# Performance work log

Measured on AMD Instinct MI355X. Metric: run time of the kernel, lower is better.

Reference implementation:

```python
import jax, jax.numpy as jnp
import numpy as np

B, D_IN, HID, LAT, K = 8192, 1024, 2048, 256, 4096

def setup_inputs() -> dict:
    key = jax.random.key(0)
    ks = jax.random.split(key, 16)
    s = lambda fan_in: 1.0 / np.sqrt(fan_in)
    inp = {
        'x':  jax.random.normal(ks[0], (B, D_IN), jnp.float32),
        # encoder MLP
        'W1': jax.random.normal(ks[1], (D_IN, HID), jnp.float32) * s(D_IN),
        'b1': jnp.zeros((HID,), jnp.float32),
        'W2': jax.random.normal(ks[2], (HID, HID), jnp.float32) * s(HID),
        'b2': jnp.zeros((HID,), jnp.float32),
        'W3': jax.random.normal(ks[3], (HID, LAT), jnp.float32) * s(HID),
        'b3': jnp.zeros((LAT,), jnp.float32),
        # codebook, uniform(-1/K, 1/K) per nn.init.uniform_
        'embed': jax.random.uniform(ks[4], (K, LAT), jnp.float32, -1.0 / K, 1.0 / K),
        # decoder MLP
        'D1': jax.random.normal(ks[5], (LAT, HID), jnp.float32) * s(LAT),
        'd1': jnp.zeros((HID,), jnp.float32),
        'D2': jax.random.normal(ks[6], (HID, HID), jnp.float32) * s(HID),
        'd2': jnp.zeros((HID,), jnp.float32),
        'D3': jax.random.normal(ks[7], (HID, D_IN), jnp.float32) * s(HID),
        'd3': jnp.zeros((D_IN,), jnp.float32),
    }
    return inp

def gelu(x):
    return jax.nn.gelu(x, approximate=False)  # torch nn.GELU default is exact erf

def reference(x, W1, b1, W2, b2, W3, b3, embed, D1, d1, D2, d2, D3, d3):
    sg = jax.lax.stop_gradient
    # encoder: [B, D_in] -> [B, latent]
    h = gelu(x @ W1 + b1)
    h = gelu(h @ W2 + b2)
    z_e = h @ W3 + b3
    # squared distances to codebook: ||z||^2 + ||e||^2 - 2 z.e -> [B, K]
    z_sq = jnp.sum(z_e * z_e, axis=1, keepdims=True)
    e_sq = jnp.sum(embed * embed, axis=1)[None, :]
    dist = z_sq + e_sq - 2.0 * (z_e @ embed.T)
    indices = jnp.argmin(dist, axis=1)            # [B]
    z_q = embed[indices]                          # [B, latent]
    commitment = jnp.mean((z_e - sg(z_q)) ** 2)
    codebook = jnp.mean((z_q - sg(z_e)) ** 2)
    vq_loss = codebook + 0.25 * commitment
    # straight-through estimator
    z_st = z_e + sg(z_q - z_e)
    # decoder: [B, latent] -> [B, D_in]
    g = gelu(z_st @ D1 + d1)
    g = gelu(g @ D2 + d2)
    x_recon = g @ D3 + d3
    return x_recon, vq_loss, indices
```

## Files before the change

kernel.cpp:

```cpp
#include <hip/hip_runtime.h>
#include <math.h>

#define B_    8192
#define DIN_  1024
#define HID_  2048
#define LAT_  256
#define KC_   4096

using bfrag8 = __attribute__((ext_vector_type(8))) short;
using short8 = __attribute__((ext_vector_type(8))) short;
using half8  = __attribute__((ext_vector_type(8))) _Float16;
using facc4  = __attribute__((ext_vector_type(4))) float;

__device__ __forceinline__ unsigned short f2bf(float f) {
    union { float f; unsigned int u; } c; c.f = f;
    unsigned int u = c.u;
    return (unsigned short)((u + 0x7FFFu + ((u >> 16) & 1u)) >> 16);
}

__device__ __forceinline__ unsigned short f2h_bits(float f) {
    union { _Float16 h; unsigned short u; } c; c.h = (_Float16)f;
    return c.u;
}

__device__ __forceinline__ void gload16(const unsigned short* g, unsigned short* l) {
    __builtin_amdgcn_global_load_lds(
        (const __attribute__((address_space(1))) void*)(g),
        (__attribute__((address_space(3))) void*)(l), 16, 0, 0);
}

template <int GELU, int OUT_SPLIT>
__global__ __launch_bounds__(256, 3) void gemm_split_f16(
    const unsigned short* __restrict__ Ahi, const unsigned short* __restrict__ Alo,
    const unsigned short* __restrict__ WThi, const unsigned short* __restrict__ WTlo,
    const float* __restrict__ bias,
    unsigned short* __restrict__ Chi, unsigned short* __restrict__ Clo,
    float* __restrict__ Cf32,
    int M, int N, int K)
{
    __shared__ __align__(16) unsigned short AsH[128 * 64];
    __shared__ __align__(16) unsigned short AsL[128 * 64];
    __shared__ __align__(16) unsigned short WsH[64 * 64];
    __shared__ __align__(16) unsigned short WsL[64 * 64];

    const int tid  = threadIdx.x;
    const int wave = tid >> 6;
    const int lane = tid & 63;
    const int wm   = wave & 1;
    const int wn   = wave >> 1;
    const int quad = lane >> 4;
    const int ln   = lane & 15;
    const int n0 = blockIdx.x * 64;
    const int m0 = blockIdx.y * 128;

    const facc4 fz4 = {0.0f, 0.0f, 0.0f, 0.0f};
    facc4 accA[4][2] = {};
    facc4 accB[4][2] = {};
    facc4 master[4][2] = {};

    for (int k0 = 0; k0 < K; k0 += 64) {
#pragma unroll
        for (int i = 0; i < 4; ++i) {
            const int idx = i * 256 + tid;
            const int row = idx >> 3;
            const int gs  = (idx & 7) ^ (row & 7);
            const int wb  = i * 256 + (tid & 192);
            const size_t src = (size_t)(m0 + row) * K + k0 + gs * 8;
            gload16(&Ahi[src], &AsH[wb * 8]);
            gload16(&Alo[src], &AsL[wb * 8]);
        }
#pragma unroll
        for (int i = 0; i < 2; ++i) {
            const int idx = i * 256 + tid;
            const int row = idx >> 3;
            const int gs  = (idx & 7) ^ (row & 7);
            const int wb  = i * 256 + (tid & 192);
            const size_t src = (size_t)(n0 + row) * K + k0 + gs * 8;
            gload16(&WThi[src], &WsH[wb * 8]);
            gload16(&WTlo[src], &WsL[wb * 8]);
        }
        __syncthreads();
#pragma unroll
        for (int ks = 0; ks < 64; ks += 32) {
            const int gq = (ks >> 3) + quad;
            half8 aH[4], aL[4], bH[2], bL[2];
#pragma unroll
            for (int f = 0; f < 4; ++f) {
                const int row = wm * 64 + f * 16 + ln;
                const int off = row * 64 + ((gq ^ (ln & 7)) << 3);
                aH[f] = *reinterpret_cast<const half8*>(&AsH[off]);
                aL[f] = *reinterpret_cast<const half8*>(&AsL[off]);
            }
#pragma unroll
            for (int f = 0; f < 2; ++f) {
                const int row = wn * 32 + f * 16 + ln;
                const int off = row * 64 + ((gq ^ (ln & 7)) << 3);
                bH[f] = *reinterpret_cast<const half8*>(&WsH[off]);
                bL[f] = *reinterpret_cast<const half8*>(&WsL[off]);
            }
#pragma unroll
            for (int fm = 0; fm < 4; ++fm)
#pragma unroll
                for (int fn = 0; fn < 2; ++fn)
                    accA[fm][fn] = __builtin_amdgcn_mfma_f32_16x16x32_f16(
                        aH[fm], bH[fn], accA[fm][fn], 0, 0, 0);
#pragma unroll
            for (int fm = 0; fm < 4; ++fm)
#pragma unroll
                for (int fn = 0; fn < 2; ++fn)
                    accB[fm][fn] = __builtin_amdgcn_mfma_f32_16x16x32_f16(
                        aH[fm], bL[fn], accB[fm][fn], 0, 0, 0);
#pragma unroll
            for (int fm = 0; fm < 4; ++fm)
#pragma unroll
                for (int fn = 0; fn < 2; ++fn)
                    accB[fm][fn] = __builtin_amdgcn_mfma_f32_16x16x32_f16(
                        aL[fm], bH[fn], accB[fm][fn], 0, 0, 0);
        }
        __syncthreads();
        if ((k0 & 192) == 192) {
#pragma unroll
            for (int fm = 0; fm < 4; ++fm)
#pragma unroll
                for (int fn = 0; fn < 2; ++fn) {
                    master[fm][fn] += accA[fm][fn];
                    accA[fm][fn] = fz4;
                }
        }
    }

    const double SC_HI = 0.015625;
    const double SC_LO = 3.814697265625e-06;
#pragma unroll
    for (int fn = 0; fn < 2; ++fn) {
        const int col = n0 + wn * 32 + fn * 16 + ln;
        const double bb = (double)bias[col];
#pragma unroll
        for (int fm = 0; fm < 4; ++fm) {
            const int rbase = m0 + wm * 64 + fm * 16 + quad * 4;
#pragma unroll
            for (int r = 0; r < 4; ++r) {
                double v = (double)master[fm][fn][r] * SC_HI
                         + (double)accB[fm][fn][r] * SC_LO + bb;
                if (GELU) v = 0.5 * v * (1.0 + erf(v * 0.70710678118654752440));
                const float hf = (float)v;
                if (OUT_SPLIT == 1 || OUT_SPLIT == 2) {
                    const _Float16 hi = (_Float16)hf;
                    const float lo = (hf - (float)hi) * 4096.0f;
                    union { _Float16 h; unsigned short u; } c1, c2;
                    c1.h = hi; c2.h = (_Float16)lo;
                    Chi[(size_t)(rbase + r) * N + col] = c1.u;
                    Clo[(size_t)(rbase + r) * N + col] = c2.u;
                }
                if (OUT_SPLIT == 0 || OUT_SPLIT == 2) {
                    Cf32[(size_t)(rbase + r) * N + col] = hf;
                }
            }
        }
    }
}

__global__ __launch_bounds__(256) void split_scaled_f16x2(
    const float* __restrict__ X, unsigned short* __restrict__ Xhi,
    unsigned short* __restrict__ Xlo, int n4, float scale)
{
    const int i = blockIdx.x * 256 + threadIdx.x;
    if (i >= n4) return;
    const float4 v = reinterpret_cast<const float4*>(X)[i];
    ushort4 h, l;
    {
        const float s = v.x * scale;
        _Float16 a = (_Float16)s; h.x = f2h_bits((float)a); l.x = f2h_bits((s - (float)a) * 4096.0f);
    }
    {
        const float s = v.y * scale;
        _Float16 a = (_Float16)s; h.y = f2h_bits((float)a); l.y = f2h_bits((s - (float)a) * 4096.0f);
    }
    {
        const float s = v.z * scale;
        _Float16 a = (_Float16)s; h.z = f2h_bits((float)a); l.z = f2h_bits((s - (float)a) * 4096.0f);
    }
    {
        const float s = v.w * scale;
        _Float16 a = (_Float16)s; h.w = f2h_bits((float)a); l.w = f2h_bits((s - (float)a) * 4096.0f);
    }
    reinterpret_cast<ushort4*>(Xhi)[i] = h;
    reinterpret_cast<ushort4*>(Xlo)[i] = l;
}

__global__ __launch_bounds__(64) void emb_prep(
    const float* __restrict__ E, float* __restrict__ esq,
    unsigned short* __restrict__ Ehi, unsigned short* __restrict__ Elo,
    float* __restrict__ loss_slot)
{
    const int r = blockIdx.x;
    const float4 v = reinterpret_cast<const float4*>(E + (size_t)r * LAT_)[threadIdx.x];
    ushort4 h, l;
    {
        const float s = v.x * 65536.0f;
        _Float16 a = (_Float16)s; h.x = f2h_bits((float)a); l.x = f2h_bits((s - (float)a) * 4096.0f);
    }
    {
        const float s = v.y * 65536.0f;
        _Float16 a = (_Float16)s; h.y = f2h_bits((float)a); l.y = f2h_bits((s - (float)a) * 4096.0f);
    }
    {
        const float s = v.z * 65536.0f;
        _Float16 a = (_Float16)s; h.z = f2h_bits((float)a); l.z = f2h_bits((s - (float)a) * 4096.0f);
    }
    {
        const float s = v.w * 65536.0f;
        _Float16 a = (_Float16)s; h.w = f2h_bits((float)a); l.w = f2h_bits((s - (float)a) * 4096.0f);
    }
    reinterpret_cast<ushort4*>(Ehi + (size_t)r * LAT_)[threadIdx.x] = h;
    reinterpret_cast<ushort4*>(Elo + (size_t)r * LAT_)[threadIdx.x] = l;
    double s = (double)v.x * v.x + (double)v.y * v.y + (double)v.z * v.z + (double)v.w * v.w;
#pragma unroll
    for (int off = 32; off; off >>= 1) s += __shfl_down(s, off, 64);
    if (threadIdx.x == 0) {
        esq[r] = (float)s;
        if (r == 0) *loss_slot = 0.0f;
    }
}

__global__ __launch_bounds__(256) void wsplit_transpose(
    const float* __restrict__ W, unsigned short* __restrict__ WThi,
    unsigned short* __restrict__ WTlo, int K, int N)
{
    __shared__ float t[32][33];
    const int k0 = blockIdx.x * 32;
    const int n0 = blockIdx.y * 32;
    const int x = threadIdx.x;
    const int y = threadIdx.y;
#pragma unroll
    for (int i = 0; i < 4; ++i)
        t[y + i * 8][x] = W[(size_t)(k0 + y + i * 8) * N + n0 + x];
    __syncthreads();
#pragma unroll
    for (int i = 0; i < 4; ++i) {
        const float w = t[x][y + i * 8] * 64.0f;
        const _Float16 hi = (_Float16)w;
        const float lo = (w - (float)hi) * 4096.0f;
        WThi[(size_t)(n0 + y + i * 8) * K + k0 + x] = f2h_bits((float)hi);
        WTlo[(size_t)(n0 + y + i * 8) * K + k0 + x] = f2h_bits(lo);
    }
}

__global__ __launch_bounds__(256, 2) void vq_argmin_mfma(
    const unsigned short* __restrict__ Zhi, const unsigned short* __restrict__ Zlo,
    const unsigned short* __restrict__ Ehi, const unsigned short* __restrict__ Elo,
    const float* __restrict__ esq, const float* __restrict__ zsq,
    float* __restrict__ pval, int* __restrict__ pidx)
{
    __shared__ __align__(16) unsigned short ZsH[128 * 64];
    __shared__ __align__(16) unsigned short ZsL[128 * 64];
    __shared__ __align__(16) unsigned short EsH[64 * 64];
    __shared__ __align__(16) unsigned short EsL[64 * 64];
    __shared__ float rbv[128][2];
    __shared__ int   rbi[128][2];

    const int tid  = threadIdx.x;
    const int wave = tid >> 6;
    const int lane = tid & 63;
    const int wm   = wave & 1;
    const int wn   = wave >> 1;
    const int quad = lane >> 4;
    const int ln   = lane & 15;
    const int m0    = blockIdx.x * 128;
    const int split = blockIdx.y;

    float zsqv[4][4];
#pragma unroll
    for (int fm = 0; fm < 4; ++fm) {
        const float4 q = *reinterpret_cast<const float4*>(
            &zsq[m0 + wm * 64 + fm * 16 + quad * 4]);
        zsqv[fm][0] = q.x; zsqv[fm][1] = q.y; zsqv[fm][2] = q.z; zsqv[fm][3] = q.w;
    }

    float bestv[4][4];
    int   besti[4][4];
#pragma unroll
    for (int a = 0; a < 4; ++a)
#pragma unroll
        for (int b = 0; b < 4; ++b) { bestv[a][b] = 3.4e38f; besti[a][b] = 0; }

    for (int nt = 0; nt < 8; ++nt) {
        const int n0 = split * 512 + nt * 64;
        facc4 accA[4][2] = {};
        facc4 accB[4][2] = {};
        for (int k0 = 0; k0 < 256; k0 += 64) {
            __syncthreads();
#pragma unroll
            for (int i = 0; i < 4; ++i) {
                const int idx = i * 256 + tid;
                const int row = idx >> 3;
                const int gs  = (idx & 7) ^ (row & 7);
                const int wb  = i * 256 + (tid & 192);
                const size_t src = (size_t)(m0 + row) * LAT_ + k0 + gs * 8;
                gload16(&Zhi[src], &ZsH[wb * 8]);
                gload16(&Zlo[src], &ZsL[wb * 8]);
            }
#pragma unroll
            for (int i = 0; i < 2; ++i) {
                const int idx = i * 256 + tid;
                const int row = idx >> 3;
                const int gs  = (idx & 7) ^ (row & 7);
                const int wb  = i * 256 + (tid & 192);
                const size_t src = (size_t)(n0 + row) * LAT_ + k0 + gs * 8;
                gload16(&Ehi[src], &EsH[wb * 8]);
                gload16(&Elo[src], &EsL[wb * 8]);
            }
            __syncthreads();
#pragma unroll
            for (int ks = 0; ks < 64; ks += 32) {
                const int gq = (ks >> 3) + quad;
                half8 aH[4], aL[4], bH[2], bL[2];
#pragma unroll
                for (int f = 0; f < 4; ++f) {
                    const int row = wm * 64 + f * 16 + ln;
                    const int off = row * 64 + ((gq ^ (ln & 7)) << 3);
                    aH[f] = *reinterpret_cast<const half8*>(&ZsH[off]);
                    aL[f] = *reinterpret_cast<const half8*>(&ZsL[off]);
                }
#pragma unroll
                for (int f = 0; f < 2; ++f) {
                    const int row = wn * 32 + f * 16 + ln;
                    const int off = row * 64 + ((gq ^ (ln & 7)) << 3);
                    bH[f] = *reinterpret_cast<const half8*>(&EsH[off]);
                    bL[f] = *reinterpret_cast<const half8*>(&EsL[off]);
                }
#pragma unroll
                for (int fm = 0; fm < 4; ++fm)
#pragma unroll
                    for (int fn = 0; fn < 2; ++fn)
                        accA[fm][fn] = __builtin_amdgcn_mfma_f32_16x16x32_f16(
                            aH[fm], bH[fn], accA[fm][fn], 0, 0, 0);
#pragma unroll
                for (int fm = 0; fm < 4; ++fm)
#pragma unroll
                    for (int fn = 0; fn < 2; ++fn)
                        accB[fm][fn] = __builtin_amdgcn_mfma_f32_16x16x32_f16(
                            aH[fm], bL[fn], accB[fm][fn], 0, 0, 0);
#pragma unroll
                for (int fm = 0; fm < 4; ++fm)
#pragma unroll
                    for (int fn = 0; fn < 2; ++fn)
                        accB[fm][fn] = __builtin_amdgcn_mfma_f32_16x16x32_f16(
                            aL[fm], bH[fn], accB[fm][fn], 0, 0, 0);
            }
        }
#pragma unroll
        for (int fm = 0; fm < 4; ++fm)
#pragma unroll
            for (int fn = 0; fn < 2; ++fn) {
                const int n = n0 + wn * 32 + fn * 16 + ln;
                const float es = esq[n];
#pragma unroll
                for (int r = 0; r < 4; ++r) {
                    const float pa = accA[fm][fn][r] * 0x1p-15f;
                    const float pb = accB[fm][fn][r] * 0x1p-27f;
                    const float t2m = pa + pb;
                    const float sc = (zsqv[fm][r] + es) - t2m;
                    if (sc < bestv[fm][r]) { bestv[fm][r] = sc; besti[fm][r] = n; }
                }
            }
    }

#pragma unroll
    for (int fm = 0; fm < 4; ++fm)
#pragma unroll
        for (int r = 0; r < 4; ++r) {
            float v0 = bestv[fm][r]; int i0 = besti[fm][r];
#pragma unroll
            for (int mask = 1; mask < 16; mask <<= 1) {
                const float v2 = __shfl_xor(v0, mask, 64);
                const int   i2 = __shfl_xor(i0, mask, 64);
                if (v2 < v0 || (v2 == v0 && i2 < i0)) { v0 = v2; i0 = i2; }
            }
            bestv[fm][r] = v0; besti[fm][r] = i0;
        }

    if (ln == 0) {
#pragma unroll
        for (int fm = 0; fm < 4; ++fm)
#pragma unroll
            for (int r = 0; r < 4; ++r) {
                const int rl = wm * 64 + fm * 16 + quad * 4 + r;
                rbv[rl][wn] = bestv[fm][r];
                rbi[rl][wn] = besti[fm][r];
            }
    }
    __syncthreads();
    if (tid < 128) {
        float bv = rbv[tid][0]; int bi = rbi[tid][0];
        const float v = rbv[tid][1]; const int ix = rbi[tid][1];
        if (v < bv || (v == bv && ix < bi)) { bv = v; bi = ix; }
        pval[(size_t)(m0 + tid) * 8 + split] = bv;
        pidx[(m0 + tid) * 8 + split] = bi;
    }
}

template <int OUT_BF16>
__global__ __launch_bounds__(256) void gemm_mfma_bf16(
    const unsigned short* __restrict__ A,
    const unsigned short* __restrict__ WT,
    const float* __restrict__ bias,
    void* __restrict__ Cout,
    int M, int N, int K)
{
    __shared__ __align__(16) unsigned short As[128 * 64];
    __shared__ __align__(16) unsigned short Bs[128 * 64];

    const int tid  = threadIdx.x;
    const int wave = tid >> 6;
    const int lane = tid & 63;
    const int wm   = wave & 1;
    const int wn   = wave >> 1;
    const int quad = lane >> 4;
    const int ln   = lane & 15;
    const int m0 = blockIdx.x * 128;
    const int n0 = blockIdx.y * 128;

    facc4 acc[4][4] = {};

    for (int k0 = 0; k0 < K; k0 += 64) {
#pragma unroll
        for (int i = 0; i < 4; ++i) {
            const int idx = i * 256 + tid;
            const int row = idx >> 3;
            const int c8  = (idx & 7) * 8;
            const int wb  = i * 256 + (tid & 192);
            gload16(&A[(size_t)(m0 + row) * K + k0 + c8], &As[wb * 8]);
            gload16(&WT[(size_t)(n0 + row) * K + k0 + c8], &Bs[wb * 8]);
        }
        __syncthreads();
#pragma unroll
        for (int ks = 0; ks < 64; ks += 32) {
            bfrag8 am[4], bn[4];
#pragma unroll
            for (int f = 0; f < 4; ++f) {
                am[f] = *reinterpret_cast<const bfrag8*>(
                    &As[(wm * 64 + f * 16 + ln) * 64 + ks + quad * 8]);
                bn[f] = *reinterpret_cast<const bfrag8*>(
                    &Bs[(wn * 64 + f * 16 + ln) * 64 + ks + quad * 8]);
            }
#pragma unroll
            for (int fm = 0; fm < 4; ++fm)
#pragma unroll
                for (int fn = 0; fn < 4; ++fn)
                    acc[fm][fn] = __builtin_amdgcn_mfma_f32_16x16x32_bf16(
                        am[fm], bn[fn], acc[fm][fn], 0, 0, 0);
        }
        __syncthreads();
    }

#pragma unroll
    for (int fn = 0; fn < 4; ++fn) {
        const int col = n0 + wn * 64 + fn * 16 + ln;
        const float bf = bias[col];
#pragma unroll
        for (int fm = 0; fm < 4; ++fm) {
            const int rbase = m0 + wm * 64 + fm * 16 + quad * 4;
#pragma unroll
            for (int r = 0; r < 4; ++r) {
                float v = acc[fm][fn][r] + bf;
                if (OUT_BF16) {
                    v = 0.5f * v * (1.0f + erff(v * 0.70710678118654752440f));
                    ((unsigned short*)Cout)[(size_t)(rbase + r) * N + col] = f2bf(v);
                } else {
                    ((float*)Cout)[(size_t)(rbase + r) * N + col] = v;
                }
            }
        }
    }
}

__global__ __launch_bounds__(256) void cast_transpose_w(
    const float* __restrict__ W, unsigned short* __restrict__ WT, int K, int N)
{
    __shared__ float t[32][33];
    const int k0 = blockIdx.x * 32;
    const int n0 = blockIdx.y * 32;
    const int x = threadIdx.x;
    const int y = threadIdx.y;
#pragma unroll
    for (int i = 0; i < 4; ++i)
        t[y + i * 8][x] = W[(size_t)(k0 + y + i * 8) * N + n0 + x];
    __syncthreads();
#pragma unroll
    for (int i = 0; i < 4; ++i)
        WT[(size_t)(n0 + y + i * 8) * K + k0 + x] = f2bf(t[x][y + i * 8]);
}

__global__ __launch_bounds__(64) void rowsq_kernel(
    const float* __restrict__ X, float* __restrict__ out,
    float* __restrict__ loss_slot)
{
    const int r = blockIdx.x;
    const float4 v = reinterpret_cast<const float4*>(X + (size_t)r * LAT_)[threadIdx.x];
    double s = (double)v.x * v.x + (double)v.y * v.y + (double)v.z * v.z + (double)v.w * v.w;
#pragma unroll
    for (int off = 32; off; off >>= 1) s += __shfl_down(s, off, 64);
    if (threadIdx.x == 0) {
        out[r] = (float)s;
        if (loss_slot != nullptr && r == 0) *loss_slot = 0.0f;
    }
}

__global__ __launch_bounds__(64) void vq_finalize(
    const float* __restrict__ pval, const int* __restrict__ pidx,
    const float* __restrict__ Z, const float* __restrict__ E,
    unsigned short* __restrict__ zqb, float* __restrict__ out_idx,
    float* __restrict__ loss_slot)
{
    const int row = blockIdx.x;
    __shared__ int sidx;
    if (threadIdx.x == 0) {
        float bv = pval[row * 8]; int bi = pidx[row * 8];
#pragma unroll
        for (int s = 1; s < 8; ++s) {
            const float v = pval[row * 8 + s]; const int ix = pidx[row * 8 + s];
            if (v < bv || (v == bv && ix < bi)) { bv = v; bi = ix; }
        }
        sidx = bi;
        out_idx[row] = (float)bi;
    }
    __syncthreads();
    const int idx = sidx;
    const float4 e = reinterpret_cast<const float4*>(E + (size_t)idx * LAT_)[threadIdx.x];
    const float4 z = reinterpret_cast<const float4*>(Z + (size_t)row * LAT_)[threadIdx.x];
    ushort4 q; q.x = f2bf(e.x); q.y = f2bf(e.y); q.z = f2bf(e.z); q.w = f2bf(e.w);
    reinterpret_cast<ushort4*>(zqb + (size_t)row * LAT_)[threadIdx.x] = q;
    const float dx = z.x - e.x, dy = z.y - e.y, dz = z.z - e.z, dw = z.w - e.w;
    float s = dx * dx + dy * dy + dz * dz + dw * dw;
#pragma unroll
    for (int off = 32; off; off >>= 1) s += __shfl_down(s, off, 64);
    if (threadIdx.x == 0)
        atomicAdd(loss_slot, s * (1.25f / ((float)B_ * (float)LAT_)));
}

extern "C" void kernel_launch(void* const* d_in, const int* in_sizes, int n_in,
                              void* d_out, int out_size, void* d_ws, size_t ws_size,
                              hipStream_t stream)
{
    const float* x   = (const float*)d_in[0];
    const float* W1  = (const float*)d_in[1];
    const float* b1  = (const float*)d_in[2];
    const float* W2  = (const float*)d_in[3];
    const float* b2  = (const float*)d_in[4];
    const float* W3  = (const float*)d_in[5];
    const float* b3  = (const float*)d_in[6];
    const float* emb = (const float*)d_in[7];
    const float* D1  = (const float*)d_in[8];
    const float* d1  = (const float*)d_in[9];
    const float* D2  = (const float*)d_in[10];
    const float* d2  = (const float*)d_in[11];
    const float* D3  = (const float*)d_in[12];
    const float* d3  = (const float*)d_in[13];
    float* out = (float*)d_out;

    char* ws = (char*)d_ws;
    const size_t MB = 1u << 20;
    unsigned short* h1hi = (unsigned short*)(ws);
    unsigned short* h1lo = (unsigned short*)(ws + 32 * MB);
    unsigned short* zehi = (unsigned short*)(ws);
    unsigned short* zelo = (unsigned short*)(ws + 4 * MB);
    unsigned short* g1b  = (unsigned short*)(ws);
    unsigned short* zqb  = (unsigned short*)(ws + 32 * MB);
    unsigned short* g2b  = (unsigned short*)(ws + 32 * MB);
    unsigned short* xhi  = (unsigned short*)(ws + 64 * MB);
    unsigned short* xlo  = (unsigned short*)(ws + 80 * MB);
    unsigned short* h2hi = (unsigned short*)(ws + 64 * MB);
    unsigned short* h2lo = (unsigned short*)(ws + 96 * MB);
    unsigned short* wt1  = (unsigned short*)(ws + 64 * MB);
    unsigned short* wt2  = (unsigned short*)(ws + 65 * MB);
    unsigned short* wt3  = (unsigned short*)(ws + 73 * MB);
    float* ze = (float*)(ws + 128 * MB);
    unsigned short* w1thi = (unsigned short*)(ws + 136 * MB);
    unsigned short* w1tlo = (unsigned short*)(ws + 140 * MB);
    unsigned short* w2thi = (unsigned short*)(ws + 136 * MB);
    unsigned short* w2tlo = (unsigned short*)(ws + 144 * MB);
    unsigned short* w3thi = (unsigned short*)(ws + 136 * MB);
    unsigned short* w3tlo = (unsigned short*)(ws + 137 * MB);
    unsigned short* ehi   = (unsigned short*)(ws + 144 * MB);
    unsigned short* elo   = (unsigned short*)(ws + 146 * MB);
    float* esq  = (float*)(ws + 152 * MB);
    float* zsq  = (float*)(ws + 152 * MB + 64 * 1024);
    float* pval = (float*)(ws + 152 * MB + 128 * 1024);
    int*   pidx = (int*)  (ws + 152 * MB + 384 * 1024);

    float* loss_slot = out + (size_t)B_ * DIN_;
    float* out_idx   = loss_slot + 1;

    split_scaled_f16x2<<<(B_ * DIN_ / 4 + 255) / 256, 256, 0, stream>>>(
        x, xhi, xlo, B_ * DIN_ / 4, 1.0f);
    wsplit_transpose<<<dim3(DIN_ / 32, HID_ / 32), dim3(32, 8), 0, stream>>>(W1, w1thi, w1tlo, DIN_, HID_);

    gemm_split_f16<1, 1><<<dim3(HID_ / 64, B_ / 128), 256, 0, stream>>>(
        xhi, xlo, w1thi, w1tlo, b1, h1hi, h1lo, nullptr, B_, HID_, DIN_);

    wsplit_transpose<<<dim3(HID_ / 32, HID_ / 32), dim3(32, 8), 0, stream>>>(W2, w2thi, w2tlo, HID_, HID_);

    gemm_split_f16<1, 1><<<dim3(HID_ / 64, B_ / 128), 256, 0, stream>>>(
        h1hi, h1lo, w2thi, w2tlo, b2, h2hi, h2lo, nullptr, B_, HID_, HID_);

    emb_prep<<<KC_, 64, 0, stream>>>(emb, esq, ehi, elo, loss_slot);
    wsplit_transpose<<<dim3(HID_ / 32, LAT_ / 32), dim3(32, 8), 0, stream>>>(W3, w3thi, w3tlo, HID_, LAT_);

    gemm_split_f16<0, 2><<<dim3(LAT_ / 64, B_ / 128), 256, 0, stream>>>(
        h2hi, h2lo, w3thi, w3tlo, b3, zehi, zelo, ze, B_, LAT_, HID_);

    rowsq_kernel<<<B_, 64, 0, stream>>>(ze, zsq, nullptr);

    cast_transpose_w<<<dim3(LAT_ / 32, HID_ / 32), dim3(32, 8), 0, stream>>>(D1, wt1, LAT_, HID_);
    cast_transpose_w<<<dim3(HID_ / 32, HID_ / 32), dim3(32, 8), 0, stream>>>(D2, wt2, HID_, HID_);
    cast_transpose_w<<<dim3(HID_ / 32, DIN_ / 32), dim3(32, 8), 0, stream>>>(D3, wt3, HID_, DIN_);

    vq_argmin_mfma<<<dim3(B_ / 128, 8), 256, 0, stream>>>(
        zehi, zelo, ehi, elo, esq, zsq, pval, pidx);
    vq_finalize<<<B_, 64, 0, stream>>>(pval, pidx, ze, emb, zqb, out_idx, loss_slot);

    gemm_mfma_bf16<1><<<dim3(B_ / 128, HID_ / 128), 256, 0, stream>>>(zqb, wt1, d1, (void*)g1b, B_, HID_, LAT_);
    gemm_mfma_bf16<1><<<dim3(B_ / 128, HID_ / 128), 256, 0, stream>>>(g1b, wt2, d2, (void*)g2b, B_, HID_, HID_);
    gemm_mfma_bf16<0><<<dim3(B_ / 128, DIN_ / 128), 256, 0, stream>>>(g2b, wt3, d3, (void*)out, B_, DIN_, HID_);
}
```

Before: 1.024 ms.

## Use 8-wave 128x128 tiles for encoder split GEMMs and merge decoder weight casts

Adds an 8-wave variant of the hi/lo split-f16 GEMM that computes a 128x128 output tile per block instead of 128x64, and uses it for the first two encoder layers. Each loaded A tile then feeds twice as many output columns, which cuts global and LDS traffic per FLOP. The cost is doubled LDS per block (64KB), which lowers the number of resident blocks per CU. Separately, the three decoder weight cast-transpose launches are merged into one kernel that dispatches on block index, removing launch overhead.

```diff
diff --git a/kernel.cpp b/kernel.cpp
--- a/kernel.cpp
+++ b/kernel.cpp
@@ -30,7 +30,7 @@
 }
 
 template <int GELU, int OUT_SPLIT>
-__global__ __launch_bounds__(256, 3) void gemm_split_f16(
+__global__ __launch_bounds__(512, 4) void gemm_split_f16_w8(
     const unsigned short* __restrict__ Ahi, const unsigned short* __restrict__ Alo,
     const unsigned short* __restrict__ WThi, const unsigned short* __restrict__ WTlo,
     const float* __restrict__ bias,
@@ -40,8 +40,8 @@
 {
     __shared__ __align__(16) unsigned short AsH[128 * 64];
     __shared__ __align__(16) unsigned short AsL[128 * 64];
-    __shared__ __align__(16) unsigned short WsH[64 * 64];
-    __shared__ __align__(16) unsigned short WsL[64 * 64];
+    __shared__ __align__(16) unsigned short WsH[128 * 64];
+    __shared__ __align__(16) unsigned short WsL[128 * 64];
 
     const int tid  = threadIdx.x;
     const int wave = tid >> 6;
@@ -50,7 +50,7 @@
     const int wn   = wave >> 1;
     const int quad = lane >> 4;
     const int ln   = lane & 15;
-    const int n0 = blockIdx.x * 64;
+    const int n0 = blockIdx.x * 128;
     const int m0 = blockIdx.y * 128;
 
     const facc4 fz4 = {0.0f, 0.0f, 0.0f, 0.0f};
@@ -60,21 +60,21 @@
 
     for (int k0 = 0; k0 < K; k0 += 64) {
 #pragma unroll
-        for (int i = 0; i < 4; ++i) {
-            const int idx = i * 256 + tid;
+        for (int i = 0; i < 2; ++i) {
+            const int idx = i * 512 + tid;
             const int row = idx >> 3;
             const int gs  = (idx & 7) ^ (row & 7);
-            const int wb  = i * 256 + (tid & 192);
+            const int wb  = i * 512 + (tid & 448);
             const size_t src = (size_t)(m0 + row) * K + k0 + gs * 8;
             gload16(&Ahi[src], &AsH[wb * 8]);
             gload16(&Alo[src], &AsL[wb * 8]);
         }
 #pragma unroll
         for (int i = 0; i < 2; ++i) {
-            const int idx = i * 256 + tid;
+            const int idx = i * 512 + tid;
             const int row = idx >> 3;
             const int gs  = (idx & 7) ^ (row & 7);
-            const int wb  = i * 256 + (tid & 192);
+            const int wb  = i * 512 + (tid & 448);
             const size_t src = (size_t)(n0 + row) * K + k0 + gs * 8;
             gload16(&WThi[src], &WsH[wb * 8]);
             gload16(&WTlo[src], &WsL[wb * 8]);
@@ -160,6 +160,137 @@
     }
 }
 
+template <int GELU, int OUT_SPLIT>
+__global__ __launch_bounds__(256, 3) void gemm_split_f16(
+    const unsigned short* __restrict__ Ahi, const unsigned short* __restrict__ Alo,
+    const unsigned short* __restrict__ WThi, const unsigned short* __restrict__ WTlo,
+    const float* __restrict__ bias,
+    unsigned short* __restrict__ Chi, unsigned short* __restrict__ Clo,
+    float* __restrict__ Cf32,
+    int M, int N, int K)
+{
+    __shared__ __align__(16) unsigned short AsH[128 * 64];
+    __shared__ __align__(16) unsigned short AsL[128 * 64];
+    __shared__ __align__(16) unsigned short WsH[64 * 64];
+    __shared__ __align__(16) unsigned short WsL[64 * 64];
+
+    const int tid  = threadIdx.x;
+    const int wave = tid >> 6;
+    const int lane = tid & 63;
+    const int wm   = wave & 1;
+    const int wn   = wave >> 1;
+    const int quad = lane >> 4;
+    const int ln   = lane & 15;
+    const int n0 = blockIdx.x * 64;
+    const int m0 = blockIdx.y * 128;
+
+    const facc4 fz4 = {0.0f, 0.0f, 0.0f, 0.0f};
+    facc4 accA[4][2] = {};
+    facc4 accB[4][2] = {};
+    facc4 master[4][2] = {};
+
+    for (int k0 = 0; k0 < K; k0 += 64) {
+#pragma unroll
+        for (int i = 0; i < 4; ++i) {
+            const int idx = i * 256 + tid;
+            const int row = idx >> 3;
+            const int gs  = (idx & 7) ^ (row & 7);
+            const int wb  = i * 256 + (tid & 192);
+            const size_t src = (size_t)(m0 + row) * K + k0 + gs * 8;
+            gload16(&Ahi[src], &AsH[wb * 8]);
+            gload16(&Alo[src], &AsL[wb * 8]);
+        }
+#pragma unroll
+        for (int i = 0; i < 2; ++i) {
+            const int idx = i * 256 + tid;
+            const int row = idx >> 3;
+            const int gs  = (idx & 7) ^ (row & 7);
+            const int wb  = i * 256 + (tid & 192);
+            const size_t src = (size_t)(n0 + row) * K + k0 + gs * 8;
+            gload16(&WThi[src], &WsH[wb * 8]);
+            gload16(&WTlo[src], &WsL[wb * 8]);
+        }
+        __syncthreads();
+#pragma unroll
+        for (int ks = 0; ks < 64; ks += 32) {
+            const int gq = (ks >> 3) + quad;
+            half8 aH[4], aL[4], bH[2], bL[2];
+#pragma unroll
+            for (int f = 0; f < 4; ++f) {
+                const int row = wm * 64 + f * 16 + ln;
+                const int off = row * 64 + ((gq ^ (ln & 7)) << 3);
+                aH[f] = *reinterpret_cast<const half8*>(&AsH[off]);
+                aL[f] = *reinterpret_cast<const half8*>(&AsL[off]);
+            }
+#pragma unroll
+            for (int f = 0; f < 2; ++f) {
+                const int row = wn * 32 + f * 16 + ln;
+                const int off = row * 64 + ((gq ^ (ln & 7)) << 3);
+                bH[f] = *reinterpret_cast<const half8*>(&WsH[off]);
+                bL[f] = *reinterpret_cast<const half8*>(&WsL[off]);
+            }
+#pragma unroll
+            for (int fm = 0; fm < 4; ++fm)
+#pragma unroll
+                for (int fn = 0; fn < 2; ++fn)
+                    accA[fm][fn] = __builtin_amdgcn_mfma_f32_16x16x32_f16(
+                        aH[fm], bH[fn], accA[fm][fn], 0, 0, 0);
+#pragma unroll
+            for (int fm = 0; fm < 4; ++fm)
+#pragma unroll
+                for (int fn = 0; fn < 2; ++fn)
+                    accB[fm][fn] = __builtin_amdgcn_mfma_f32_16x16x32_f16(
+                        aH[fm], bL[fn], accB[fm][fn], 0, 0, 0);
+#pragma unroll
+            for (int fm = 0; fm < 4; ++fm)
+#pragma unroll
+                for (int fn = 0; fn < 2; ++fn)
+                    accB[fm][fn] = __builtin_amdgcn_mfma_f32_16x16x32_f16(
+                        aL[fm], bH[fn], accB[fm][fn], 0, 0, 0);
+        }
+        __syncthreads();
+        if ((k0 & 192) == 192) {
+#pragma unroll
+            for (int fm = 0; fm < 4; ++fm)
+#pragma unroll
+                for (int fn = 0; fn < 2; ++fn) {
+                    master[fm][fn] += accA[fm][fn];
+                    accA[fm][fn] = fz4;
+                }
+        }
+    }
+
+    const double SC_HI = 0.015625;
+    const double SC_LO = 3.814697265625e-06;
+#pragma unroll
+    for (int fn = 0; fn < 2; ++fn) {
+        const int col = n0 + wn * 32 + fn * 16 + ln;
+        const double bb = (double)bias[col];
+#pragma unroll
+        for (int fm = 0; fm < 4; ++fm) {
+            const int rbase = m0 + wm * 64 + fm * 16 + quad * 4;
+#pragma unroll
+            for (int r = 0; r < 4; ++r) {
+                double v = (double)master[fm][fn][r] * SC_HI
+                         + (double)accB[fm][fn][r] * SC_LO + bb;
+                if (GELU) v = 0.5 * v * (1.0 + erf(v * 0.70710678118654752440));
+                const float hf = (float)v;
+                if (OUT_SPLIT == 1 || OUT_SPLIT == 2) {
+                    const _Float16 hi = (_Float16)hf;
+                    const float lo = (hf - (float)hi) * 4096.0f;
+                    union { _Float16 h; unsigned short u; } c1, c2;
+                    c1.h = hi; c2.h = (_Float16)lo;
+                    Chi[(size_t)(rbase + r) * N + col] = c1.u;
+                    Clo[(size_t)(rbase + r) * N + col] = c2.u;
+                }
+                if (OUT_SPLIT == 0 || OUT_SPLIT == 2) {
+                    Cf32[(size_t)(rbase + r) * N + col] = hf;
+                }
+            }
+        }
+    }
+}
+
 __global__ __launch_bounds__(256) void split_scaled_f16x2(
     const float* __restrict__ X, unsigned short* __restrict__ Xhi,
     unsigned short* __restrict__ Xlo, int n4, float scale)
@@ -475,12 +606,20 @@
     }
 }
 
-__global__ __launch_bounds__(256) void cast_transpose_w(
-    const float* __restrict__ W, unsigned short* __restrict__ WT, int K, int N)
-{
+__global__ __launch_bounds__(256) void cast_transpose_w3(
+    const float* __restrict__ D1w, unsigned short* __restrict__ wt1,
+    const float* __restrict__ D2w, unsigned short* __restrict__ wt2,
+    const float* __restrict__ D3w, unsigned short* __restrict__ wt3)
+{
+    const int bid = blockIdx.x;
+    const float* W; unsigned short* WT; int K, N, kt, nt;
+    if (bid < 512)        { W = D1w; WT = wt1; K = LAT_; N = HID_; kt = bid & 7;  nt = bid >> 3; }
+    else if (bid < 4608)  { const int l = bid - 512;  W = D2w; WT = wt2; K = HID_; N = HID_; kt = l & 63; nt = l >> 6; }
+    else                  { const int l = bid - 4608; W = D3w; WT = wt3; K = HID_; N = DIN_; kt = l & 63; nt = l >> 6; }
+
     __shared__ float t[32][33];
-    const int k0 = blockIdx.x * 32;
-    const int n0 = blockIdx.y * 32;
+    const int k0 = kt * 32;
+    const int n0 = nt * 32;
     const int x = threadIdx.x;
     const int y = threadIdx.y;
 #pragma unroll
@@ -596,12 +735,12 @@
         x, xhi, xlo, B_ * DIN_ / 4, 1.0f);
     wsplit_transpose<<<dim3(DIN_ / 32, HID_ / 32), dim3(32, 8), 0, stream>>>(W1, w1thi, w1tlo, DIN_, HID_);
 
-    gemm_split_f16<1, 1><<<dim3(HID_ / 64, B_ / 128), 256, 0, stream>>>(
+    gemm_split_f16_w8<1, 1><<<dim3(HID_ / 128, B_ / 128), 512, 0, stream>>>(
         xhi, xlo, w1thi, w1tlo, b1, h1hi, h1lo, nullptr, B_, HID_, DIN_);
 
     wsplit_transpose<<<dim3(HID_ / 32, HID_ / 32), dim3(32, 8), 0, stream>>>(W2, w2thi, w2tlo, HID_, HID_);
 
-    gemm_split_f16<1, 1><<<dim3(HID_ / 64, B_ / 128), 256, 0, stream>>>(
+    gemm_split_f16_w8<1, 1><<<dim3(HID_ / 128, B_ / 128), 512, 0, stream>>>(
         h1hi, h1lo, w2thi, w2tlo, b2, h2hi, h2lo, nullptr, B_, HID_, HID_);
 
     emb_prep<<<KC_, 64, 0, stream>>>(emb, esq, ehi, elo, loss_slot);
@@ -612,9 +751,7 @@
 
     rowsq_kernel<<<B_, 64, 0, stream>>>(ze, zsq, nullptr);
 
-    cast_transpose_w<<<dim3(LAT_ / 32, HID_ / 32), dim3(32, 8), 0, stream>>>(D1, wt1, LAT_, HID_);
-    cast_transpose_w<<<dim3(HID_ / 32, HID_ / 32), dim3(32, 8), 0, stream>>>(D2, wt2, HID_, HID_);
-    cast_transpose_w<<<dim3(HID_ / 32, DIN_ / 32), dim3(32, 8), 0, stream>>>(D3, wt3, HID_, DIN_);
+    cast_transpose_w3<<<6656, dim3(32, 8), 0, stream>>>(D1, wt1, D2, wt2, D3, wt3);
 
     vq_argmin_mfma<<<dim3(B_ / 128, 8), 256, 0, stream>>>(
         zehi, zelo, ehi, elo, esq, zsq, pval, pidx);
```

Result: slower. 1.134 ms (+10.8%).

## Swizzle workgroup IDs across XCDs and merge decoder weight cast kernels

Applied to the files above, without the earlier changes.

Adds an XCD-aware remapping of the linear block index in the split-f16 GEMM, the VQ argmin kernel and the bf16 GEMM, so that neighbouring tiles that share operand rows or columns land on the same XCD and its L2 cache. Raises the VQ argmin occupancy hint from 2 to 3 blocks per CU, and fuses the three decoder weight cast-transpose launches into one flat-grid kernel to cut launch overhead. The swizzle assumes the block count is a multiple of 8, and the higher occupancy hint may force register spilling.

```diff
diff --git a/kernel.cpp b/kernel.cpp
--- a/kernel.cpp
+++ b/kernel.cpp
@@ -27,6 +27,10 @@
     __builtin_amdgcn_global_load_lds(
         (const __attribute__((address_space(1))) void*)(g),
         (__attribute__((address_space(3))) void*)(l), 16, 0, 0);
+}
+
+__device__ __forceinline__ unsigned int xcd_swz(unsigned int lin, unsigned int nwg) {
+    return (lin & 7u) * (nwg >> 3) + (lin >> 3);
 }
 
 template <int GELU, int OUT_SPLIT>
@@ -50,8 +54,11 @@
     const int wn   = wave >> 1;
     const int quad = lane >> 4;
     const int ln   = lane & 15;
-    const int n0 = blockIdx.x * 64;
-    const int m0 = blockIdx.y * 128;
+
+    const unsigned int gx  = gridDim.x;
+    const unsigned int nl  = xcd_swz(blockIdx.y * gx + blockIdx.x, gx * gridDim.y);
+    const int n0 = (int)(nl % gx) * 64;
+    const int m0 = (int)(nl / gx) * 128;
 
     const facc4 fz4 = {0.0f, 0.0f, 0.0f, 0.0f};
     facc4 accA[4][2] = {};
@@ -246,7 +253,7 @@
     }
 }
 
-__global__ __launch_bounds__(256, 2) void vq_argmin_mfma(
+__global__ __launch_bounds__(256, 3) void vq_argmin_mfma(
     const unsigned short* __restrict__ Zhi, const unsigned short* __restrict__ Zlo,
     const unsigned short* __restrict__ Ehi, const unsigned short* __restrict__ Elo,
     const float* __restrict__ esq, const float* __restrict__ zsq,
@@ -266,8 +273,10 @@
     const int wn   = wave >> 1;
     const int quad = lane >> 4;
     const int ln   = lane & 15;
-    const int m0    = blockIdx.x * 128;
-    const int split = blockIdx.y;
+
+    const unsigned int nl = xcd_swz(blockIdx.y * 64 + blockIdx.x, 512);
+    const int m0    = (int)(nl & 63u) * 128;
+    const int split = (int)(nl >> 6);
 
     float zsqv[4][4];
 #pragma unroll
@@ -418,8 +427,11 @@
     const int wn   = wave >> 1;
     const int quad = lane >> 4;
     const int ln   = lane & 15;
-    const int m0 = blockIdx.x * 128;
-    const int n0 = blockIdx.y * 128;
+
+    const unsigned int gx  = gridDim.x;
+    const unsigned int nl  = xcd_swz(blockIdx.y * gx + blockIdx.x, gx * gridDim.y);
+    const int m0 = (int)(nl % gx) * 128;
+    const int n0 = (int)(nl / gx) * 128;
 
     facc4 acc[4][4] = {};
 
@@ -475,12 +487,20 @@
     }
 }
 
-__global__ __launch_bounds__(256) void cast_transpose_w(
-    const float* __restrict__ W, unsigned short* __restrict__ WT, int K, int N)
-{
+__global__ __launch_bounds__(256) void cast_transpose_w3(
+    const float* __restrict__ D1w, unsigned short* __restrict__ wt1,
+    const float* __restrict__ D2w, unsigned short* __restrict__ wt2,
+    const float* __restrict__ D3w, unsigned short* __restrict__ wt3)
+{
+    const int bid = blockIdx.x;
+    const float* W; unsigned short* WT; int K, N, kt, nt;
+    if (bid < 512)        { W = D1w; WT = wt1; K = LAT_; N = HID_; kt = bid & 7;  nt = bid >> 3; }
+    else if (bid < 4608)  { const int l = bid - 512;  W = D2w; WT = wt2; K = HID_; N = HID_; kt = l & 63; nt = l >> 6; }
+    else                  { const int l = bid - 4608; W = D3w; WT = wt3; K = HID_; N = DIN_; kt = l & 63; nt = l >> 6; }
+
     __shared__ float t[32][33];
-    const int k0 = blockIdx.x * 32;
-    const int n0 = blockIdx.y * 32;
+    const int k0 = kt * 32;
+    const int n0 = nt * 32;
     const int x = threadIdx.x;
     const int y = threadIdx.y;
 #pragma unroll
@@ -612,9 +632,7 @@
 
     rowsq_kernel<<<B_, 64, 0, stream>>>(ze, zsq, nullptr);
 
-    cast_transpose_w<<<dim3(LAT_ / 32, HID_ / 32), dim3(32, 8), 0, stream>>>(D1, wt1, LAT_, HID_);
-    cast_transpose_w<<<dim3(HID_ / 32, HID_ / 32), dim3(32, 8), 0, stream>>>(D2, wt2, HID_, HID_);
-    cast_transpose_w<<<dim3(HID_ / 32, DIN_ / 32), dim3(32, 8), 0, stream>>>(D3, wt3, HID_, DIN_);
+    cast_transpose_w3<<<6656, dim3(32, 8), 0, stream>>>(D1, wt1, D2, wt2, D3, wt3);
 
     vq_argmin_mfma<<<dim3(B_ / 128, 8), 256, 0, stream>>>(
         zehi, zelo, ehi, elo, esq, zsq, pval, pidx);
```

After: 1.076 ms. +5.1%, slower.
